# Performance work log

Measured on AMD Instinct MI355X. Metric: run time of the kernel, lower is better.

The kernel has to match this reference:

```python
import jax, jax.numpy as jnp
import numpy as np

MARGIN = 5.0
VAR_FLOOR = 1e-4
BIG = 1e6


def setup_inputs() -> dict:
    key = jax.random.key(0)
    ks = jax.random.split(key, 8)
    B, D, R = 512, 768, 128
    C_new, C_old = 10, 100
    return {
        "features": jax.random.normal(ks[0], (B, D), jnp.float32),
        "labels": jax.random.randint(ks[1], (B,), 0, C_new),
        "new_class_ids": jnp.arange(C_new),
        "cur_means": jax.random.normal(ks[2], (C_new, D), jnp.float32),
        "cur_bases": jax.random.normal(ks[3], (C_new, D, R), jnp.float32),
        "cur_variances": jax.random.uniform(ks[4], (C_new, R + 1), jnp.float32),
        "calibrated_old_means": jax.random.normal(ks[5], (C_old, D), jnp.float32),
        "calibrated_old_bases": jax.random.normal(ks[6], (C_old, D, R), jnp.float32),
        "calibrated_old_variances": jax.random.uniform(ks[7], (C_old, R + 1), jnp.float32),
    }


def _geometry_distance_matrix(z, means, bases, variances):
    # z: [B,D], means: [C,D], bases: [C,D,R], variances: [C,R+1] -> [B,C]
    diff = z[:, None, :] - means[None, :, :]                    # [B,C,D]
    coeff = jnp.einsum('bcd,cdr->bcr', diff, bases)             # [B,C,R]
    eig = jnp.maximum(variances[:, :-1], VAR_FLOOR)             # [C,R]
    res = jnp.maximum(variances[:, -1], VAR_FLOOR)              # [C]
    parallel = jnp.sum(coeff * coeff / eig[None, :, :], axis=-1)  # [B,C]
    recon = jnp.einsum('bcr,cdr->bcd', coeff, bases)            # [B,C,D]
    residual_term = jnp.sum((diff - recon) ** 2, axis=-1) / res[None, :]
    dist = (parallel + residual_term) / z.shape[1]              # normalize_by_dim
    return jnp.nan_to_num(dist, nan=BIG, posinf=BIG, neginf=BIG)


def reference(features, labels, new_class_ids, cur_means, cur_bases, cur_variances,
              calibrated_old_means, calibrated_old_bases, calibrated_old_variances):
    z = jnp.nan_to_num(features, nan=0.0, posinf=0.0, neginf=0.0)  # [B,D]
    labels = labels.reshape(-1)

    own_all = _geometry_distance_matrix(z, cur_means, cur_bases, cur_variances)  # [B,C_new_total]
    old_all = _geometry_distance_matrix(z, calibrated_old_means, calibrated_old_bases,
                                        calibrated_old_variances)               # [B,C_old]
    old_min = jnp.min(old_all, axis=1)                                           # [B]

    # Per-new-class masks; union of class masks reproduces new_mask implicitly.
    masks = (labels[None, :] == new_class_ids[:, None]).astype(z.dtype)          # [K,B]
    counts = masks.sum(axis=1)                                                   # [K]
    denom = jnp.maximum(counts, 1.0)

    own_k = own_all[:, new_class_ids].T                                          # [K,B]
    hinge = jax.nn.relu(MARGIN + own_k - old_min[None, :])                       # [K,B]

    total_k = (hinge * masks).sum(axis=1) / denom
    own_k_mean = (own_k * masks).sum(axis=1) / denom
    old_k_mean = (old_min[None, :] * masks).sum(axis=1) / denom

    valid = (counts > 0).astype(z.dtype)
    n_valid = jnp.maximum(valid.sum(), 1.0)
    total = (total_k * valid).sum() / n_valid
    own = (own_k_mean * valid).sum() / n_valid
    old = (old_k_mean * valid).sum() / n_valid
    return jnp.stack([total, own, old])  # [total, own, old]
```

## Files before the change

kernel.cpp:

```cpp
#include <hip/hip_runtime.h>
#include <hip/hip_bf16.h>
#include <math.h>
#include <stdint.h>

#define B_N   512
#define D_N   768
#define R_N   128
#define C_NEW 10
#define C_OLD 100
#define C_TOT 110
#define MARGIN_F    5.0f
#define VAR_FLOOR_F 1e-4f
#define BIG_F       1e6f

typedef __bf16 bf16;
typedef __bf16 bf16x4 __attribute__((ext_vector_type(4)));
typedef __bf16 bf16x8 __attribute__((ext_vector_type(8)));
typedef float  f32x4  __attribute__((ext_vector_type(4)));

__device__ __forceinline__ float cleanf(float v) { return isfinite(v) ? v : 0.0f; }

__device__ __forceinline__ unsigned encf(float f) {
    unsigned u = __float_as_uint(f);
    return (u & 0x80000000u) ? ~u : (u | 0x80000000u);
}
__device__ __forceinline__ float decf(unsigned u) {
    return (u & 0x80000000u) ? __uint_as_float(u & 0x7fffffffu) : __uint_as_float(~u);
}

__global__ __launch_bounds__(256)
void prep_T(const float* __restrict__ cur_bases, const float* __restrict__ old_bases,
            bf16* __restrict__ basesT, unsigned* __restrict__ ominE)
{
    const int bid = blockIdx.x, t = threadIdx.x;
    if (bid == 0) {
        ominE[t] = 0xFFFFFFFFu;
        ominE[256 + t] = 0xFFFFFFFFu;
    }

    const int dt = bid % 6, c = bid / 6;
    const float* Bc = (c < C_NEW) ? cur_bases + (size_t)c * D_N * R_N
                                  : old_bases + (size_t)(c - C_NEW) * D_N * R_N;
    __shared__ bf16 T[128][128];
    const int d0 = dt * 128;
    const int rg  = t & 31;
    const int dgb = t >> 5;

    #pragma unroll
    for (int i = 0; i < 4; ++i) {
        const int dg = i * 8 + dgb;
        const float* src = Bc + (size_t)(d0 + dg * 4) * R_N + rg * 4;
        float4 v0 = *(const float4*)(src);
        float4 v1 = *(const float4*)(src + R_N);
        float4 v2 = *(const float4*)(src + 2 * R_N);
        float4 v3 = *(const float4*)(src + 3 * R_N);
        const float* f0 = (const float*)&v0;
        const float* f1 = (const float*)&v1;
        const float* f2 = (const float*)&v2;
        const float* f3 = (const float*)&v3;
        #pragma unroll
        for (int j = 0; j < 4; ++j) {
            const int R = rg * 4 + j;
            const int pc = dg ^ (R & 31);
            bf16x4 w;
            w[0] = (bf16)f0[j]; w[1] = (bf16)f1[j]; w[2] = (bf16)f2[j]; w[3] = (bf16)f3[j];
            *(bf16x4*)(&T[R][pc * 4]) = w;
        }
    }
    __syncthreads();

    #pragma unroll
    for (int it = 0; it < 16; ++it) {
        const int q = it * 256 + t;
        const int r = q >> 5, u = q & 31;
        const int pc = u ^ (r & 31);
        ushort4 w = *(const ushort4*)(&T[r][pc * 4]);
        *(ushort4*)(basesT + (size_t)c * R_N * D_N + (size_t)r * D_N + d0 + u * 4) = w;
    }
}

#define PADC 136
#define SM_A   0
#define SM_B   18432
#define SM_C   0
#define SM_G   36864
#define SM_MU  71680
#define SM_INV 74752
#define SM_Q   75264
#define SM_PAR 75776
#define SM_CN  76288
#define SM_ND  76800
#define SM_T2  77312
#define SM_SZ  79360

__global__ __launch_bounds__(256, 2)
void main_all(const float* __restrict__ z, const bf16* __restrict__ basesT,
              const float* __restrict__ cur_vars, const float* __restrict__ old_vars,
              const float* __restrict__ cur_means, const float* __restrict__ old_means,
              float* __restrict__ gdist, unsigned* __restrict__ ominE)
{
    const int fid = blockIdx.x;
    const int c  = (fid & 7) + 8 * (fid >> 5);
    const int mt = (fid >> 3) & 3;
    if (c >= C_TOT) return;

    __shared__ __align__(16) unsigned char smem[SM_SZ];
    bf16*  sA   = (bf16*)(smem + SM_A);
    bf16*  sB   = (bf16*)(smem + SM_B);
    bf16*  sC   = (bf16*)(smem + SM_C);
    bf16*  sG   = (bf16*)(smem + SM_G);
    float* sMu  = (float*)(smem + SM_MU);
    float* sInv = (float*)(smem + SM_INV);
    float* sQ   = (float*)(smem + SM_Q);
    float* sPar = (float*)(smem + SM_PAR);
    float* sCn  = (float*)(smem + SM_CN);
    float* sNd  = (float*)(smem + SM_ND);
    float* sT2  = (float*)(smem + SM_T2);

    const int tid = threadIdx.x, wave = tid >> 6, lane = tid & 63;
    const int quad = lane >> 4, l15 = lane & 15;
    const int wr = (wave >> 1) * 64, wc = (wave & 1) * 64;

    const int b0 = mt * 128;
    const float* vars = (c < C_NEW) ? cur_vars + (size_t)c * (R_N + 1)
                                    : old_vars + (size_t)(c - C_NEW) * (R_N + 1);
    const float* mu = (c < C_NEW) ? cur_means + (size_t)c * D_N
                                  : old_means + (size_t)(c - C_NEW) * D_N;

    if (tid < 128) {
        sInv[tid] = 1.0f / fmaxf(vars[tid], VAR_FLOOR_F);
        sQ[tid] = 0.0f;
    }
    for (int i = tid; i < D_N; i += 256) sMu[i] = mu[i];

    const int srow = (tid * 8) >> 6 , dummy = srow;
    (void)dummy;
    const int qrow = tid >> 3 << 0;
    (void)qrow;

    const bf16* Bb = basesT + (size_t)c * R_N * D_N;
    const float* Az = z + (size_t)b0 * D_N;
    const int rb = tid >> 4, f4 = tid & 15;

    f32x4 accG[4][4];
    #pragma unroll
    for (int i = 0; i < 4; ++i)
        #pragma unroll
        for (int j = 0; j < 4; ++j) accG[i][j] = (f32x4)0.0f;

    uint4 pb[4];
    #pragma unroll
    for (int p = 0; p < 4; ++p) {
        int q = p * 256 + tid, row = q >> 3, u = q & 7;
        pb[p] = *(const uint4*)(Bb + (size_t)row * D_N + 0 + u * 8);
    }

    for (int kc = 0; kc < 12; ++kc) {
        __syncthreads();
        #pragma unroll
        for (int p = 0; p < 4; ++p) {
            int q = p * 256 + tid, row = q >> 3, u = q & 7;
            *(uint4*)(sB + row * 72 + u * 8) = pb[p];
        }
        if (kc < 11) {
            #pragma unroll
            for (int p = 0; p < 4; ++p) {
                int q = p * 256 + tid, row = q >> 3, u = q & 7;
                pb[p] = *(const uint4*)(Bb + (size_t)row * D_N + (kc + 1) * 64 + u * 8);
            }
        }
        __syncthreads();
        #pragma unroll
        for (int kk = 0; kk < 64; kk += 32) {
            bf16x8 afB[4], bgB[4];
            #pragma unroll
            for (int i = 0; i < 4; ++i) afB[i] = *(const bf16x8*)(sB + (wr + 16 * i + l15) * 72 + kk + quad * 8);
            #pragma unroll
            for (int j = 0; j < 4; ++j) bgB[j] = *(const bf16x8*)(sB + (wc + 16 * j + l15) * 72 + kk + quad * 8);
            #pragma unroll
            for (int i = 0; i < 4; ++i)
                #pragma unroll
                for (int j = 0; j < 4; ++j)
                    accG[i][j] = __builtin_amdgcn_mfma_f32_16x16x32_bf16(afB[i], bgB[j], accG[i][j], 0, 0, 0);
        }
    }
    #pragma unroll
    for (int i = 0; i < 4; ++i)
        #pragma unroll
        for (int j = 0; j < 4; ++j)
            #pragma unroll
            for (int reg = 0; reg < 4; ++reg)
                sG[(wr + 16 * i + quad * 4 + reg) * PADC + wc + 16 * j + l15] = (bf16)accG[i][j][reg];

    f32x4 acc1[4][4];
    #pragma unroll
    for (int i = 0; i < 4; ++i)
        #pragma unroll
        for (int j = 0; j < 4; ++j) acc1[i][j] = (f32x4)0.0f;
    float nd2p[8];
    #pragma unroll
    for (int p = 0; p < 8; ++p) nd2p[p] = 0.f;

    float4 pa[8];
    #pragma unroll
    for (int p = 0; p < 4; ++p) {
        int q = p * 256 + tid, row = q >> 3, u = q & 7;
        pb[p] = *(const uint4*)(Bb + (size_t)row * D_N + 0 + u * 8);
    }
    #pragma unroll
    for (int p = 0; p < 8; ++p) {
        int row = p * 16 + rb;
        pa[p] = *(const float4*)(Az + (size_t)row * D_N + 0 + f4 * 4);
    }

    for (int kc = 0; kc < 12; ++kc) {
        const int k0 = kc * 64;
        __syncthreads();
        #pragma unroll
        for (int p = 0; p < 4; ++p) {
            int q = p * 256 + tid, row = q >> 3, u = q & 7;
            *(uint4*)(sB + row * 72 + u * 8) = pb[p];
        }
        {
            float4 m4 = *(const float4*)(sMu + k0 + f4 * 4);
            #pragma unroll
            for (int p = 0; p < 8; ++p) {
                int row = p * 16 + rb;
                float d0 = cleanf(pa[p].x) - m4.x;
                float d1 = cleanf(pa[p].y) - m4.y;
                float d2 = cleanf(pa[p].z) - m4.z;
                float d3 = cleanf(pa[p].w) - m4.w;
                nd2p[p] += d0 * d0 + d1 * d1 + d2 * d2 + d3 * d3;
                bf16x4 w;
                w[0] = (bf16)d0; w[1] = (bf16)d1; w[2] = (bf16)d2; w[3] = (bf16)d3;
                *(bf16x4*)(sA + row * 72 + f4 * 4) = w;
            }
        }
        if (kc < 11) {
            #pragma unroll
            for (int p = 0; p < 4; ++p) {
                int q = p * 256 + tid, row = q >> 3, u = q & 7;
                pb[p] = *(const uint4*)(Bb + (size_t)row * D_N + (kc + 1) * 64 + u * 8);
            }
            #pragma unroll
            for (int p = 0; p < 8; ++p) {
                int row = p * 16 + rb;
                pa[p] = *(const float4*)(Az + (size_t)row * D_N + (kc + 1) * 64 + f4 * 4);
            }
        }
        __syncthreads();
        #pragma unroll
        for (int kk = 0; kk < 64; kk += 32) {
            bf16x8 afA[4], bgB[4];
            #pragma unroll
            for (int i = 0; i < 4; ++i) afA[i] = *(const bf16x8*)(sA + (wr + 16 * i + l15) * 72 + kk + quad * 8);
            #pragma unroll
            for (int j = 0; j < 4; ++j) bgB[j] = *(const bf16x8*)(sB + (wc + 16 * j + l15) * 72 + kk + quad * 8);
            #pragma unroll
            for (int i = 0; i < 4; ++i)
                #pragma unroll
                for (int j = 0; j < 4; ++j)
                    acc1[i][j] = __builtin_amdgcn_mfma_f32_16x16x32_bf16(afA[i], bgB[j], acc1[i][j], 0, 0, 0);
        }
    }

    #pragma unroll
    for (int p = 0; p < 8; ++p) {
        float s = nd2p[p];
        s += __shfl_xor(s, 1, 64); s += __shfl_xor(s, 2, 64);
        s += __shfl_xor(s, 4, 64); s += __shfl_xor(s, 8, 64);
        if (l15 == 0) sNd[p * 16 + rb] = s;
    }
    __syncthreads();

    #pragma unroll
    for (int i = 0; i < 4; ++i)
        #pragma unroll
        for (int j = 0; j < 4; ++j)
            #pragma unroll
            for (int reg = 0; reg < 4; ++reg)
                sC[(wr + 16 * i + quad * 4 + reg) * PADC + wc + 16 * j + l15] = (bf16)acc1[i][j][reg];
    __syncthreads();

    {
        int row = tid >> 1, half = tid & 1;
        float par = 0.f, cn = 0.f;
        #pragma unroll
        for (int m = 0; m < 8; ++m) {
            bf16x8 v = *(const bf16x8*)(sC + row * PADC + half * 64 + m * 8);
            #pragma unroll
            for (int e = 0; e < 8; ++e) {
                float f = (float)v[e];
                int col = half * 64 + m * 8 + e;
                cn  += f * f;
                par += f * f * sInv[col];
            }
        }
        sT2[tid] = par;
        sT2[256 + tid] = cn;
    }
    __syncthreads();
    if (tid < 128) {
        sPar[tid] = sT2[tid * 2] + sT2[tid * 2 + 1];
        sCn[tid]  = sT2[256 + tid * 2] + sT2[256 + tid * 2 + 1];
    }

    f32x4 acc2[4][4];
    #pragma unroll
    for (int i = 0; i < 4; ++i)
        #pragma unroll
        for (int j = 0; j < 4; ++j) acc2[i][j] = (f32x4)0.0f;
    #pragma unroll
    for (int kc = 0; kc < 128; kc += 32) {
        bf16x8 af[4], bg[4];
        #pragma unroll
        for (int i = 0; i < 4; ++i) af[i] = *(const bf16x8*)(sC + (wr + 16 * i + l15) * PADC + kc + quad * 8);
        #pragma unroll
        for (int j = 0; j < 4; ++j) bg[j] = *(const bf16x8*)(sG + (wc + 16 * j + l15) * PADC + kc + quad * 8);
        #pragma unroll
        for (int i = 0; i < 4; ++i)
            #pragma unroll
            for (int j = 0; j < 4; ++j)
                acc2[i][j] = __builtin_amdgcn_mfma_f32_16x16x32_bf16(af[i], bg[j], acc2[i][j], 0, 0, 0);
    }

    #pragma unroll
    for (int i = 0; i < 4; ++i)
        #pragma unroll
        for (int reg = 0; reg < 4; ++reg) {
            float qp = 0.f;
            #pragma unroll
            for (int j = 0; j < 4; ++j) qp += acc2[i][j][reg] * acc1[i][j][reg];
            qp += __shfl_xor(qp, 1, 64);
            qp += __shfl_xor(qp, 2, 64);
            qp += __shfl_xor(qp, 4, 64);
            qp += __shfl_xor(qp, 8, 64);
            if (l15 == 0) atomicAdd(&sQ[wr + 16 * i + quad * 4 + reg], qp);
        }
    __syncthreads();

    if (tid < 128) {
        int b = b0 + tid;
        float res = fmaxf(vars[R_N], VAR_FLOOR_F);
        float dist = (sPar[tid] + (sNd[tid] - 2.0f * sCn[tid] + sQ[tid]) / res) / (float)D_N;
        if (!isfinite(dist)) dist = BIG_F;
        if (c < C_NEW) {
            gdist[(size_t)b * C_NEW + c] = dist;
        } else {
            atomicMin(ominE + b, encf(dist));
        }
    }
}

__global__ __launch_bounds__(512)
void finalize(const float* __restrict__ gdist, const unsigned* __restrict__ ominE,
              const int* __restrict__ labels, const int* __restrict__ ncid,
              float* __restrict__ out)
{
    __shared__ float acc[C_NEW * 4];
    __shared__ int sNcid[C_NEW];
    const int t = threadIdx.x;
    if (t < C_NEW * 4) acc[t] = 0.f;
    if (t < C_NEW) sNcid[t] = ncid[t];
    __syncthreads();

    {
        float mn = decf(ominE[t]);
        const int lab = labels[t];
        #pragma unroll
        for (int k = 0; k < C_NEW; ++k) {
            if (lab == sNcid[k]) {
                int col = min(max(sNcid[k], 0), C_NEW - 1);
                float ow = gdist[(size_t)t * C_NEW + col];
                atomicAdd(&acc[k * 4 + 0], 1.0f);
                atomicAdd(&acc[k * 4 + 1], fmaxf(0.0f, MARGIN_F + ow - mn));
                atomicAdd(&acc[k * 4 + 2], ow);
                atomicAdd(&acc[k * 4 + 3], mn);
            }
        }
    }
    __syncthreads();

    if (t == 0) {
        float total = 0.f, own = 0.f, old = 0.f, nv = 0.f;
        #pragma unroll
        for (int k = 0; k < C_NEW; ++k) {
            float cnt = acc[k * 4 + 0];
            float den = fmaxf(cnt, 1.0f);
            if (cnt > 0.f) {
                nv += 1.f;
                total += acc[k * 4 + 1] / den;
                own   += acc[k * 4 + 2] / den;
                old   += acc[k * 4 + 3] / den;
            }
        }
        float nvd = fmaxf(nv, 1.0f);
        out[0] = total / nvd;
        out[1] = own / nvd;
        out[2] = old / nvd;
    }
}

extern "C" void kernel_launch(void* const* d_in, const int* in_sizes, int n_in,
                              void* d_out, int out_size, void* d_ws, size_t ws_size,
                              hipStream_t stream)
{
    const float* features  = (const float*)d_in[0];
    const int*   labels    = (const int*)d_in[1];
    const int*   ncid      = (const int*)d_in[2];
    const float* cur_means = (const float*)d_in[3];
    const float* cur_bases = (const float*)d_in[4];
    const float* cur_vars  = (const float*)d_in[5];
    const float* old_means = (const float*)d_in[6];
    const float* old_bases = (const float*)d_in[7];
    const float* old_vars  = (const float*)d_in[8];

    unsigned char* ws = (unsigned char*)d_ws;
    float*    gdist  = (float*)(ws + 0);
    unsigned* ominE  = (unsigned*)(ws + 20480);
    bf16*     basesT = (bf16*) (ws + 22528);

    prep_T<<<dim3(6 * C_TOT), dim3(256), 0, stream>>>(cur_bases, old_bases,
                                                      basesT, ominE);
    main_all<<<dim3(448), dim3(256), 0, stream>>>(features, basesT,
                                                  cur_vars, old_vars,
                                                  cur_means, old_means,
                                                  gdist, ominE);
    finalize<<<dim3(1), dim3(512), 0, stream>>>(gdist, ominE, labels, ncid,
                                                (float*)d_out);
}
```

Measured before the change: 186.5 us.

## Precompute per-class Gram matrices in prep kernel and halve main-kernel batch tile

The 128x128 Gram matrix B^T B for each class moves out of the main kernel, where each of the four batch tiles recomputed it, into extra blocks of the prep kernel that write it to global memory once. The main kernel now uses 64-row batch tiles with a smaller LDS footprint, a higher occupancy target and twice as many blocks. It reads G directly from global memory for the second MFMA and re-reads the coefficients from LDS instead of keeping them in registers. In exchange, register prefetch of bases and features is dropped, the basis tiles are streamed twice as many times, and the prep kernel carries extra Gram work.

New measurement: 158.8 us. 1.17x faster.

```diff
diff --git a/kernel.cpp b/kernel.cpp
--- a/kernel.cpp
+++ b/kernel.cpp
@@ -28,20 +28,101 @@
     return (u & 0x80000000u) ? __uint_as_float(u & 0x7fffffffu) : __uint_as_float(~u);
 }
 
-__global__ __launch_bounds__(256)
-void prep_T(const float* __restrict__ cur_bases, const float* __restrict__ old_bases,
-            bf16* __restrict__ basesT, unsigned* __restrict__ ominE)
+__global__ __launch_bounds__(256, 2)
+void prep_gram(const float* __restrict__ cur_bases, const float* __restrict__ old_bases,
+               bf16* __restrict__ basesT, bf16* __restrict__ G,
+               unsigned* __restrict__ ominE)
 {
     const int bid = blockIdx.x, t = threadIdx.x;
-    if (bid == 0) {
-        ominE[t] = 0xFFFFFFFFu;
-        ominE[256 + t] = 0xFFFFFFFFu;
-    }
-
-    const int dt = bid % 6, c = bid / 6;
+    __shared__ __align__(16) unsigned char lds[32768 + 512];
+
+    if (bid < C_TOT) {
+        if (bid == 0) {
+            ominE[t] = 0xFFFFFFFFu;
+            ominE[256 + t] = 0xFFFFFFFFu;
+        }
+        const int c = bid;
+        const float* Bc = (c < C_NEW) ? cur_bases + (size_t)c * D_N * R_N
+                                      : old_bases + (size_t)(c - C_NEW) * D_N * R_N;
+        bf16* sT = (bf16*)lds;
+        const int wave = t >> 6, lane = t & 63;
+        const int quad = lane >> 4, l15 = lane & 15;
+        const int wrg = (wave >> 1) * 64, wsg = (wave & 1) * 64;
+        const int rg = t & 31, dgq = t >> 5;
+
+        f32x4 acc[4][4];
+        #pragma unroll
+        for (int i = 0; i < 4; ++i)
+            #pragma unroll
+            for (int j = 0; j < 4; ++j) acc[i][j] = (f32x4)0.0f;
+
+        float4 pf[8];
+        #pragma unroll
+        for (int i = 0; i < 2; ++i) {
+            const int dg = i * 8 + dgq;
+            const float* src = Bc + (size_t)(dg * 4) * R_N + rg * 4;
+            #pragma unroll
+            for (int m = 0; m < 4; ++m) pf[i * 4 + m] = *(const float4*)(src + m * R_N);
+        }
+
+        for (int kc = 0; kc < 12; ++kc) {
+            __syncthreads();
+            #pragma unroll
+            for (int i = 0; i < 2; ++i) {
+                const int dg = i * 8 + dgq;
+                #pragma unroll
+                for (int j = 0; j < 4; ++j) {
+                    const int R = rg * 4 + j;
+                    bf16x4 w;
+                    w[0] = (bf16)pf[i * 4 + 0][j];
+                    w[1] = (bf16)pf[i * 4 + 1][j];
+                    w[2] = (bf16)pf[i * 4 + 2][j];
+                    w[3] = (bf16)pf[i * 4 + 3][j];
+                    *(bf16x4*)(sT + R * 72 + dg * 4) = w;
+                }
+            }
+            if (kc < 11) {
+                #pragma unroll
+                for (int i = 0; i < 2; ++i) {
+                    const int dg = i * 8 + dgq;
+                    const float* src = Bc + (size_t)((kc + 1) * 64 + dg * 4) * R_N + rg * 4;
+                    #pragma unroll
+                    for (int m = 0; m < 4; ++m) pf[i * 4 + m] = *(const float4*)(src + m * R_N);
+                }
+            }
+            __syncthreads();
+            #pragma unroll
+            for (int kk = 0; kk < 64; kk += 32) {
+                bf16x8 af[4], bg[4];
+                #pragma unroll
+                for (int i = 0; i < 4; ++i) af[i] = *(const bf16x8*)(sT + (wrg + 16 * i + l15) * 72 + kk + quad * 8);
+                #pragma unroll
+                for (int j = 0; j < 4; ++j) bg[j] = *(const bf16x8*)(sT + (wsg + 16 * j + l15) * 72 + kk + quad * 8);
+                #pragma unroll
+                for (int i = 0; i < 4; ++i)
+                    #pragma unroll
+                    for (int j = 0; j < 4; ++j)
+                        acc[i][j] = __builtin_amdgcn_mfma_f32_16x16x32_bf16(af[i], bg[j], acc[i][j], 0, 0, 0);
+            }
+        }
+        #pragma unroll
+        for (int i = 0; i < 4; ++i)
+            #pragma unroll
+            for (int j = 0; j < 4; ++j)
+                #pragma unroll
+                for (int reg = 0; reg < 4; ++reg) {
+                    int r = wrg + 16 * i + quad * 4 + reg;
+                    int s = wsg + 16 * j + l15;
+                    G[(size_t)c * 16384 + (size_t)r * 128 + s] = (bf16)acc[i][j][reg];
+                }
+        return;
+    }
+
+    const int tb = bid - C_TOT;
+    const int dt = tb % 6, c = tb / 6;
     const float* Bc = (c < C_NEW) ? cur_bases + (size_t)c * D_N * R_N
                                   : old_bases + (size_t)(c - C_NEW) * D_N * R_N;
-    __shared__ bf16 T[128][128];
+    bf16 (*T)[128] = (bf16(*)[128])lds;
     const int d0 = dt * 128;
     const int rg  = t & 31;
     const int dgb = t >> 5;
@@ -80,35 +161,36 @@
 }
 
 #define PADC 136
-#define SM_A   0
-#define SM_B   18432
-#define SM_C   0
-#define SM_G   36864
-#define SM_MU  71680
-#define SM_INV 74752
-#define SM_Q   75264
-#define SM_PAR 75776
-#define SM_CN  76288
-#define SM_ND  76800
-#define SM_T2  77312
-#define SM_SZ  79360
-
-__global__ __launch_bounds__(256, 2)
-void main_all(const float* __restrict__ z, const bf16* __restrict__ basesT,
-              const float* __restrict__ cur_vars, const float* __restrict__ old_vars,
-              const float* __restrict__ cur_means, const float* __restrict__ old_means,
-              float* __restrict__ gdist, unsigned* __restrict__ ominE)
+#define SM_A    0
+#define SM_B    9216
+#define SM_C    0
+#define SM_MU   27648
+#define SM_INV  30720
+#define SM_Q    31232
+#define SM_PAR  31488
+#define SM_CN   31744
+#define SM_ND   32000
+#define SM_T2   32256
+#define SM_SZ   34304
+
+__global__ __launch_bounds__(256, 4)
+void main_dist(const float* __restrict__ z, const bf16* __restrict__ basesT,
+               const bf16* __restrict__ G,
+               const float* __restrict__ cur_vars, const float* __restrict__ old_vars,
+               const float* __restrict__ cur_means, const float* __restrict__ old_means,
+               float* __restrict__ gdist, unsigned* __restrict__ ominE)
 {
     const int fid = blockIdx.x;
-    const int c  = (fid & 7) + 8 * (fid >> 5);
-    const int mt = (fid >> 3) & 3;
+    const int x = fid & 7;
+    const int y = (fid % 112) >> 3;
+    const int mt = fid / 112;
+    const int c = x + 8 * y;
     if (c >= C_TOT) return;
 
     __shared__ __align__(16) unsigned char smem[SM_SZ];
     bf16*  sA   = (bf16*)(smem + SM_A);
     bf16*  sB   = (bf16*)(smem + SM_B);
     bf16*  sC   = (bf16*)(smem + SM_C);
-    bf16*  sG   = (bf16*)(smem + SM_G);
     float* sMu  = (float*)(smem + SM_MU);
     float* sInv = (float*)(smem + SM_INV);
     float* sQ   = (float*)(smem + SM_Q);
@@ -119,99 +201,31 @@
 
     const int tid = threadIdx.x, wave = tid >> 6, lane = tid & 63;
     const int quad = lane >> 4, l15 = lane & 15;
-    const int wr = (wave >> 1) * 64, wc = (wave & 1) * 64;
-
-    const int b0 = mt * 128;
+    const int wr  = (wave >> 1) * 32;
+    const int wcc = (wave & 1) * 64;
+
+    const int b0 = mt * 64;
     const float* vars = (c < C_NEW) ? cur_vars + (size_t)c * (R_N + 1)
                                     : old_vars + (size_t)(c - C_NEW) * (R_N + 1);
     const float* mu = (c < C_NEW) ? cur_means + (size_t)c * D_N
                                   : old_means + (size_t)(c - C_NEW) * D_N;
 
-    if (tid < 128) {
-        sInv[tid] = 1.0f / fmaxf(vars[tid], VAR_FLOOR_F);
-        sQ[tid] = 0.0f;
-    }
+    if (tid < 128) sInv[tid] = 1.0f / fmaxf(vars[tid], VAR_FLOOR_F);
+    if (tid < 64)  sQ[tid] = 0.0f;
     for (int i = tid; i < D_N; i += 256) sMu[i] = mu[i];
 
-    const int srow = (tid * 8) >> 6 , dummy = srow;
-    (void)dummy;
-    const int qrow = tid >> 3 << 0;
-    (void)qrow;
-
-    const bf16* Bb = basesT + (size_t)c * R_N * D_N;
+    f32x4 acc1[2][4];
+    #pragma unroll
+    for (int i = 0; i < 2; ++i)
+        #pragma unroll
+        for (int j = 0; j < 4; ++j) acc1[i][j] = (f32x4)0.0f;
+    float nd2p[4];
+    #pragma unroll
+    for (int p = 0; p < 4; ++p) nd2p[p] = 0.f;
+
+    const int rg4 = tid >> 4, f4 = tid & 15;
     const float* Az = z + (size_t)b0 * D_N;
-    const int rb = tid >> 4, f4 = tid & 15;
-
-    f32x4 accG[4][4];
-    #pragma unroll
-    for (int i = 0; i < 4; ++i)
-        #pragma unroll
-        for (int j = 0; j < 4; ++j) accG[i][j] = (f32x4)0.0f;
-
-    uint4 pb[4];
-    #pragma unroll
-    for (int p = 0; p < 4; ++p) {
-        int q = p * 256 + tid, row = q >> 3, u = q & 7;
-        pb[p] = *(const uint4*)(Bb + (size_t)row * D_N + 0 + u * 8);
-    }
-
-    for (int kc = 0; kc < 12; ++kc) {
-        __syncthreads();
-        #pragma unroll
-        for (int p = 0; p < 4; ++p) {
-            int q = p * 256 + tid, row = q >> 3, u = q & 7;
-            *(uint4*)(sB + row * 72 + u * 8) = pb[p];
-        }
-        if (kc < 11) {
-            #pragma unroll
-            for (int p = 0; p < 4; ++p) {
-                int q = p * 256 + tid, row = q >> 3, u = q & 7;
-                pb[p] = *(const uint4*)(Bb + (size_t)row * D_N + (kc + 1) * 64 + u * 8);
-            }
-        }
-        __syncthreads();
-        #pragma unroll
-        for (int kk = 0; kk < 64; kk += 32) {
-            bf16x8 afB[4], bgB[4];
-            #pragma unroll
-            for (int i = 0; i < 4; ++i) afB[i] = *(const bf16x8*)(sB + (wr + 16 * i + l15) * 72 + kk + quad * 8);
-            #pragma unroll
-            for (int j = 0; j < 4; ++j) bgB[j] = *(const bf16x8*)(sB + (wc + 16 * j + l15) * 72 + kk + quad * 8);
-            #pragma unroll
-            for (int i = 0; i < 4; ++i)
-                #pragma unroll
-                for (int j = 0; j < 4; ++j)
-                    accG[i][j] = __builtin_amdgcn_mfma_f32_16x16x32_bf16(afB[i], bgB[j], accG[i][j], 0, 0, 0);
-        }
-    }
-    #pragma unroll
-    for (int i = 0; i < 4; ++i)
-        #pragma unroll
-        for (int j = 0; j < 4; ++j)
-            #pragma unroll
-            for (int reg = 0; reg < 4; ++reg)
-                sG[(wr + 16 * i + quad * 4 + reg) * PADC + wc + 16 * j + l15] = (bf16)accG[i][j][reg];
-
-    f32x4 acc1[4][4];
-    #pragma unroll
-    for (int i = 0; i < 4; ++i)
-        #pragma unroll
-        for (int j = 0; j < 4; ++j) acc1[i][j] = (f32x4)0.0f;
-    float nd2p[8];
-    #pragma unroll
-    for (int p = 0; p < 8; ++p) nd2p[p] = 0.f;
-
-    float4 pa[8];
-    #pragma unroll
-    for (int p = 0; p < 4; ++p) {
-        int q = p * 256 + tid, row = q >> 3, u = q & 7;
-        pb[p] = *(const uint4*)(Bb + (size_t)row * D_N + 0 + u * 8);
-    }
-    #pragma unroll
-    for (int p = 0; p < 8; ++p) {
-        int row = p * 16 + rb;
-        pa[p] = *(const float4*)(Az + (size_t)row * D_N + 0 + f4 * 4);
-    }
+    const bf16*  Bb = basesT + (size_t)c * R_N * D_N;
 
     for (int kc = 0; kc < 12; ++kc) {
         const int k0 = kc * 64;
@@ -219,79 +233,68 @@
         #pragma unroll
         for (int p = 0; p < 4; ++p) {
             int q = p * 256 + tid, row = q >> 3, u = q & 7;
-            *(uint4*)(sB + row * 72 + u * 8) = pb[p];
+            *(uint4*)(sB + row * 72 + u * 8) = *(const uint4*)(Bb + (size_t)row * D_N + k0 + u * 8);
         }
         {
             float4 m4 = *(const float4*)(sMu + k0 + f4 * 4);
             #pragma unroll
-            for (int p = 0; p < 8; ++p) {
-                int row = p * 16 + rb;
-                float d0 = cleanf(pa[p].x) - m4.x;
-                float d1 = cleanf(pa[p].y) - m4.y;
-                float d2 = cleanf(pa[p].z) - m4.z;
-                float d3 = cleanf(pa[p].w) - m4.w;
+            for (int p = 0; p < 4; ++p) {
+                int row = p * 16 + rg4;
+                float4 v = *(const float4*)(Az + (size_t)row * D_N + k0 + f4 * 4);
+                float d0 = cleanf(v.x) - m4.x;
+                float d1 = cleanf(v.y) - m4.y;
+                float d2 = cleanf(v.z) - m4.z;
+                float d3 = cleanf(v.w) - m4.w;
                 nd2p[p] += d0 * d0 + d1 * d1 + d2 * d2 + d3 * d3;
                 bf16x4 w;
                 w[0] = (bf16)d0; w[1] = (bf16)d1; w[2] = (bf16)d2; w[3] = (bf16)d3;
                 *(bf16x4*)(sA + row * 72 + f4 * 4) = w;
             }
         }
-        if (kc < 11) {
-            #pragma unroll
-            for (int p = 0; p < 4; ++p) {
-                int q = p * 256 + tid, row = q >> 3, u = q & 7;
-                pb[p] = *(const uint4*)(Bb + (size_t)row * D_N + (kc + 1) * 64 + u * 8);
-            }
-            #pragma unroll
-            for (int p = 0; p < 8; ++p) {
-                int row = p * 16 + rb;
-                pa[p] = *(const float4*)(Az + (size_t)row * D_N + (kc + 1) * 64 + f4 * 4);
-            }
-        }
         __syncthreads();
         #pragma unroll
         for (int kk = 0; kk < 64; kk += 32) {
-            bf16x8 afA[4], bgB[4];
-            #pragma unroll
-            for (int i = 0; i < 4; ++i) afA[i] = *(const bf16x8*)(sA + (wr + 16 * i + l15) * 72 + kk + quad * 8);
-            #pragma unroll
-            for (int j = 0; j < 4; ++j) bgB[j] = *(const bf16x8*)(sB + (wc + 16 * j + l15) * 72 + kk + quad * 8);
-            #pragma unroll
-            for (int i = 0; i < 4; ++i)
+            bf16x8 af[2], bg[4];
+            #pragma unroll
+            for (int i = 0; i < 2; ++i) af[i] = *(const bf16x8*)(sA + (wr + 16 * i + l15) * 72 + kk + quad * 8);
+            #pragma unroll
+            for (int j = 0; j < 4; ++j) bg[j] = *(const bf16x8*)(sB + (wcc + 16 * j + l15) * 72 + kk + quad * 8);
+            #pragma unroll
+            for (int i = 0; i < 2; ++i)
                 #pragma unroll
                 for (int j = 0; j < 4; ++j)
-                    acc1[i][j] = __builtin_amdgcn_mfma_f32_16x16x32_bf16(afA[i], bgB[j], acc1[i][j], 0, 0, 0);
-        }
-    }
-
-    #pragma unroll
-    for (int p = 0; p < 8; ++p) {
+                    acc1[i][j] = __builtin_amdgcn_mfma_f32_16x16x32_bf16(af[i], bg[j], acc1[i][j], 0, 0, 0);
+        }
+    }
+
+    #pragma unroll
+    for (int p = 0; p < 4; ++p) {
         float s = nd2p[p];
         s += __shfl_xor(s, 1, 64); s += __shfl_xor(s, 2, 64);
         s += __shfl_xor(s, 4, 64); s += __shfl_xor(s, 8, 64);
-        if (l15 == 0) sNd[p * 16 + rb] = s;
-    }
-    __syncthreads();
-
-    #pragma unroll
-    for (int i = 0; i < 4; ++i)
+        if (f4 == 0) sNd[p * 16 + rg4] = s;
+    }
+    __syncthreads();
+
+    #pragma unroll
+    for (int i = 0; i < 2; ++i)
         #pragma unroll
         for (int j = 0; j < 4; ++j)
             #pragma unroll
             for (int reg = 0; reg < 4; ++reg)
-                sC[(wr + 16 * i + quad * 4 + reg) * PADC + wc + 16 * j + l15] = (bf16)acc1[i][j][reg];
+                sC[(wr + 16 * i + quad * 4 + reg) * PADC + wcc + 16 * j + l15] = (bf16)acc1[i][j][reg];
     __syncthreads();
 
     {
-        int row = tid >> 1, half = tid & 1;
+        int row = tid >> 2, qtr = tid & 3;
         float par = 0.f, cn = 0.f;
         #pragma unroll
-        for (int m = 0; m < 8; ++m) {
-            bf16x8 v = *(const bf16x8*)(sC + row * PADC + half * 64 + m * 8);
+        for (int m = 0; m < 4; ++m) {
+            bf16x8 v = *(const bf16x8*)(sC + row * PADC + qtr * 32 + m * 8);
             #pragma unroll
             for (int e = 0; e < 8; ++e) {
                 float f = (float)v[e];
-                int col = half * 64 + m * 8 + e;
+                int col = qtr * 32 + m * 8 + e;
                 cn  += f * f;
                 par += f * f * sInv[col];
             }
@@ -300,46 +303,51 @@
         sT2[256 + tid] = cn;
     }
     __syncthreads();
-    if (tid < 128) {
-        sPar[tid] = sT2[tid * 2] + sT2[tid * 2 + 1];
-        sCn[tid]  = sT2[256 + tid * 2] + sT2[256 + tid * 2 + 1];
-    }
-
-    f32x4 acc2[4][4];
-    #pragma unroll
-    for (int i = 0; i < 4; ++i)
+    if (tid < 64) {
+        sPar[tid] = sT2[tid * 4] + sT2[tid * 4 + 1] + sT2[tid * 4 + 2] + sT2[tid * 4 + 3];
+        sCn[tid]  = sT2[256 + tid * 4] + sT2[256 + tid * 4 + 1]
+                  + sT2[256 + tid * 4 + 2] + sT2[256 + tid * 4 + 3];
+    }
+
+    const bf16* Gc = G + (size_t)c * 16384;
+    f32x4 acc2[2][4];
+    #pragma unroll
+    for (int i = 0; i < 2; ++i)
         #pragma unroll
         for (int j = 0; j < 4; ++j) acc2[i][j] = (f32x4)0.0f;
     #pragma unroll
-    for (int kc = 0; kc < 128; kc += 32) {
-        bf16x8 af[4], bg[4];
-        #pragma unroll
-        for (int i = 0; i < 4; ++i) af[i] = *(const bf16x8*)(sC + (wr + 16 * i + l15) * PADC + kc + quad * 8);
-        #pragma unroll
-        for (int j = 0; j < 4; ++j) bg[j] = *(const bf16x8*)(sG + (wc + 16 * j + l15) * PADC + kc + quad * 8);
-        #pragma unroll
-        for (int i = 0; i < 4; ++i)
+    for (int kc4 = 0; kc4 < 4; ++kc4) {
+        const int kb = kc4 * 32;
+        bf16x8 af[2], bg[4];
+        #pragma unroll
+        for (int i = 0; i < 2; ++i) af[i] = *(const bf16x8*)(sC + (wr + 16 * i + l15) * PADC + kb + quad * 8);
+        #pragma unroll
+        for (int j = 0; j < 4; ++j) bg[j] = *(const bf16x8*)(Gc + (size_t)(wcc + 16 * j + l15) * 128 + kb + quad * 8);
+        #pragma unroll
+        for (int i = 0; i < 2; ++i)
             #pragma unroll
             for (int j = 0; j < 4; ++j)
                 acc2[i][j] = __builtin_amdgcn_mfma_f32_16x16x32_bf16(af[i], bg[j], acc2[i][j], 0, 0, 0);
     }
 
     #pragma unroll
-    for (int i = 0; i < 4; ++i)
+    for (int i = 0; i < 2; ++i)
         #pragma unroll
         for (int reg = 0; reg < 4; ++reg) {
+            const int row = wr + 16 * i + quad * 4 + reg;
             float qp = 0.f;
             #pragma unroll
-            for (int j = 0; j < 4; ++j) qp += acc2[i][j][reg] * acc1[i][j][reg];
+            for (int j = 0; j < 4; ++j)
+                qp += acc2[i][j][reg] * (float)sC[row * PADC + wcc + 16 * j + l15];
             qp += __shfl_xor(qp, 1, 64);
             qp += __shfl_xor(qp, 2, 64);
             qp += __shfl_xor(qp, 4, 64);
             qp += __shfl_xor(qp, 8, 64);
-            if (l15 == 0) atomicAdd(&sQ[wr + 16 * i + quad * 4 + reg], qp);
-        }
-    __syncthreads();
-
-    if (tid < 128) {
+            if (l15 == 0) atomicAdd(&sQ[row], qp);
+        }
+    __syncthreads();
+
+    if (tid < 64) {
         int b = b0 + tid;
         float res = fmaxf(vars[R_N], VAR_FLOOR_F);
         float dist = (sPar[tid] + (sNd[tid] - 2.0f * sCn[tid] + sQ[tid]) / res) / (float)D_N;
@@ -419,13 +427,14 @@
     float*    gdist  = (float*)(ws + 0);
     unsigned* ominE  = (unsigned*)(ws + 20480);
     bf16*     basesT = (bf16*) (ws + 22528);
-
-    prep_T<<<dim3(6 * C_TOT), dim3(256), 0, stream>>>(cur_bases, old_bases,
-                                                      basesT, ominE);
-    main_all<<<dim3(448), dim3(256), 0, stream>>>(features, basesT,
-                                                  cur_vars, old_vars,
-                                                  cur_means, old_means,
-                                                  gdist, ominE);
+    bf16*     G      = (bf16*) (ws + 21649408);
+
+    prep_gram<<<dim3(C_TOT + 6 * C_TOT), dim3(256), 0, stream>>>(
+        cur_bases, old_bases, basesT, G, ominE);
+    main_dist<<<dim3(896), dim3(256), 0, stream>>>(features, basesT, G,
+                                                   cur_vars, old_vars,
+                                                   cur_means, old_means,
+                                                   gdist, ominE);
     finalize<<<dim3(1), dim3(512), 0, stream>>>(gdist, ominE, labels, ncid,
                                                 (float*)d_out);
 }
```
